# Kernel optimization log

Hardware: AMD Instinct MI355X
Metric: run time of the kernel (lower is better)

Reference implementation:

```python
import jax, jax.numpy as jnp
import numpy as np

N = 40000        # total nodes (2000 graphs x 20 nodes)
E = 60000        # edges per relation (before self-loops)
R = 6            # number of relations
IN = 32
HID = 128
OUT = 128
H = 2            # heads
C = 128          # per-head out channels (concat=False)
B = 2000         # number of graphs
NEG_SLOPE = 0.2


def setup_inputs() -> dict:
    key = jax.random.key(0)
    ks = jax.random.split(key, 16)
    rn = lambda k, s, sc=0.05: (jax.random.normal(k, s, jnp.float32) * sc)
    x = jax.random.normal(ks[0], (N, IN), jnp.float32)
    edge_index = jax.random.randint(ks[1], (R, 2, E), 0, N, dtype=jnp.int32)
    batch = (jnp.arange(N, dtype=jnp.int32) // (N // B)).astype(jnp.int32)
    return {
        "x": x, "edge_index": edge_index, "batch": batch,
        "Wl1": rn(ks[2], (R, IN, H * C)), "bl1": jnp.zeros((R, H * C), jnp.float32),
        "Wr1": rn(ks[3], (R, IN, H * C)), "br1": jnp.zeros((R, H * C), jnp.float32),
        "att1": rn(ks[4], (R, H, C)), "bias1": jnp.zeros((R, C), jnp.float32),
        "Wl2": rn(ks[5], (R, HID, H * C)), "bl2": jnp.zeros((R, H * C), jnp.float32),
        "Wr2": rn(ks[6], (R, HID, H * C)), "br2": jnp.zeros((R, H * C), jnp.float32),
        "att2": rn(ks[7], (R, H, C)), "bias2": jnp.zeros((R, C), jnp.float32),
        "ln1_g": jnp.ones((HID,), jnp.float32), "ln1_b": jnp.zeros((HID,), jnp.float32),
        "ln2_g": jnp.ones((HID,), jnp.float32), "ln2_b": jnp.zeros((HID,), jnp.float32),
        "query": rn(ks[8], (HID,), 0.02),
        "projW": rn(ks[9], (HID, OUT)), "projb": jnp.zeros((OUT,), jnp.float32),
    }


def _gatv2(x, src, dst, Wl, bl, Wr, br, att, bias):
    # x: [N, F]; src/dst: [Etot] (self-loops already appended)
    n = x.shape[0]
    xl = (x @ Wl + bl).reshape(n, H, C)   # source transform
    xr = (x @ Wr + br).reshape(n, H, C)   # target transform
    e = jax.nn.leaky_relu(xl[src] + xr[dst], NEG_SLOPE)   # [Etot, H, C]
    logits = jnp.einsum('ehc,hc->eh', e, att)             # [Etot, H]
    m = jax.ops.segment_max(logits, dst, num_segments=n)
    a = jnp.exp(logits - m[dst])
    s = jax.ops.segment_sum(a, dst, num_segments=n)
    w = a / s[dst]                                        # segment softmax
    out = jax.ops.segment_sum(w[:, :, None] * xl[src], dst, num_segments=n)
    return out.mean(axis=1) + bias                        # head-average (concat=False)


def _hetero_layer(x, edge_index, Wl, bl, Wr, br, att, bias):
    loops = jnp.broadcast_to(jnp.arange(N, dtype=edge_index.dtype), (R, N))
    src = jnp.concatenate([edge_index[:, 0, :], loops], axis=1)  # [R, E+N]
    dst = jnp.concatenate([edge_index[:, 1, :], loops], axis=1)
    outs = jax.vmap(_gatv2, in_axes=(None, 0, 0, 0, 0, 0, 0, 0, 0))(
        x, src, dst, Wl, bl, Wr, br, att, bias)
    return outs.sum(axis=0)  # HeteroConv aggr='sum'


def _layernorm(x, g, b, eps=1e-5):
    mu = x.mean(-1, keepdims=True)
    var = ((x - mu) ** 2).mean(-1, keepdims=True)
    return (x - mu) * jax.lax.rsqrt(var + eps) * g + b


def reference(x, edge_index, batch, Wl1, bl1, Wr1, br1, att1, bias1,
              Wl2, bl2, Wr2, br2, att2, bias2,
              ln1_g, ln1_b, ln2_g, ln2_b, query, projW, projb):
    h = _hetero_layer(x, edge_index, Wl1, bl1, Wr1, br1, att1, bias1)
    h = _layernorm(jnp.tanh(h), ln1_g, ln1_b)
    h = _hetero_layer(h, edge_index, Wl2, bl2, Wr2, br2, att2, bias2)
    h = _layernorm(jnp.tanh(h), ln2_g, ln2_b)
    # attention pooling over graphs (segment softmax on batch ids)
    scores = h @ query                              # [N]
    m = jax.ops.segment_max(scores, batch, num_segments=B)
    a = jnp.exp(scores - m[batch])
    s = jax.ops.segment_sum(a, batch, num_segments=B)
    w = a / s[batch]
    g = jax.ops.segment_sum(w[:, None] * h, batch, num_segments=B)  # [B, HID]
    return g @ projW + projb
```

## Files before the change

kernel.cpp:

```cpp
#include <hip/hip_runtime.h>
#include <hip/hip_bf16.h>
#include <math.h>

#define N_NODES 40000
#define E_EDGES 60000
#define R_REL 6
#define IN_F 32
#define HID_F 128
#define B_GRAPHS 2000
#define NODES_PER_G 20
#define NEG_SLOPE 0.2f
#define NB (R_REL * N_NODES)
#define NTOT (R_REL * (E_EDGES + N_NODES))
#define NBLK ((NB + 255) / 256)

#define CNT_B ((NTOT + 255) / 256)
#define CVT_B ((N_NODES * 16 + 255) / 256)
#define P1_B  (R_REL * 512 * 32 / 256)
#define P2_B  (R_REL * 512 * 128 / 256)
#define PREP_TOTAL (CNT_B + CVT_B + P1_B + P2_B + 1)

typedef __bf16 bf16x8 __attribute__((ext_vector_type(8)));
typedef float f32x4 __attribute__((ext_vector_type(4)));

__device__ __forceinline__ unsigned f2bfbits(float f) {
    unsigned u = __builtin_bit_cast(unsigned, f);
    return (u + 0x7FFFu + ((u >> 16) & 1u)) >> 16;
}
__device__ __forceinline__ float bflo(unsigned u) { return __builtin_bit_cast(float, u << 16); }
__device__ __forceinline__ float bfhi(unsigned u) { return __builtin_bit_cast(float, u & 0xFFFF0000u); }

__device__ __forceinline__ float fast_tanh(float x) {
    float e = __builtin_amdgcn_exp2f(x * 2.8853900817779268f);
    return fmaf(-2.f, __builtin_amdgcn_rcpf(e + 1.f), 1.f);
}

__device__ __forceinline__ void prep_w_body(
    const float* __restrict__ Wl, const float* __restrict__ Wr,
    const float* __restrict__ bl, const float* __restrict__ br,
    unsigned short* __restrict__ Bt, float* __restrict__ bcat, int K, int idx)
{
    if (idx >= R_REL * 512 * K) return;
    int k = idx % K;
    int rn = idx / K;
    int n = rn % 512;
    int r = rn / 512;
    int nn = n & 255;
    const float* W = (n < 256) ? Wl : Wr;
    float w = W[((size_t)r * K + k) * 256 + nn];
    Bt[idx] = (unsigned short)f2bfbits(w);
    if (k == 0)
        bcat[rn] = (n < 256) ? bl[r * 256 + nn] : br[r * 256 + nn];
}

__global__ __launch_bounds__(256) void fused_prep_kernel(
    const int* __restrict__ ei, int* __restrict__ cnt,
    const float* __restrict__ x, unsigned* __restrict__ xbf,
    const float* __restrict__ Wl1, const float* __restrict__ Wr1,
    const float* __restrict__ bl1, const float* __restrict__ br1,
    unsigned short* __restrict__ Bt1, float* __restrict__ bc1,
    const float* __restrict__ Wl2, const float* __restrict__ Wr2,
    const float* __restrict__ bl2, const float* __restrict__ br2,
    unsigned short* __restrict__ Bt2, float* __restrict__ bc2,
    const float* __restrict__ bias1, const float* __restrict__ bias2,
    float* __restrict__ bsum1, float* __restrict__ bsum2,
    const float* __restrict__ att1, const float* __restrict__ att2,
    float* __restrict__ attP1, float* __restrict__ attP2)
{
    int b = blockIdx.x;
    int tid = threadIdx.x;
    if (b < CNT_B) {
        int idx = b * 256 + tid;
        if (idx >= NTOT) return;
        int bin;
        if (idx < R_REL * E_EDGES) {
            int r = idx / E_EDGES, e = idx - r * E_EDGES;
            bin = r * N_NODES + ei[(size_t)r * 2 * E_EDGES + E_EDGES + e];
        } else {
            bin = idx - R_REL * E_EDGES;
        }
        atomicAdd(&cnt[bin], 1);
    } else if (b < CNT_B + CVT_B) {
        int i = (b - CNT_B) * 256 + tid;
        if (i >= N_NODES * 16) return;
        float2 v = *(const float2*)(x + 2 * i);
        xbf[i] = f2bfbits(v.x) | (f2bfbits(v.y) << 16);
    } else if (b < CNT_B + CVT_B + P1_B) {
        prep_w_body(Wl1, Wr1, bl1, br1, Bt1, bc1, 32, (b - CNT_B - CVT_B) * 256 + tid);
    } else if (b < CNT_B + CVT_B + P1_B + P2_B) {
        prep_w_body(Wl2, Wr2, bl2, br2, Bt2, bc2, 128, (b - CNT_B - CVT_B - P1_B) * 256 + tid);
    } else {
        const float L2E = 1.4426950408889634f;
        for (int r = 0; r < R_REL; r++) {
            float a1 = att1[r * 256 + tid];
            float a2 = att2[r * 256 + tid];
            attP1[r * 512 + tid]       = 0.6f * L2E * a1;
            attP1[r * 512 + 256 + tid] = 0.4f * L2E * a1;
            attP2[r * 512 + tid]       = 0.6f * L2E * a2;
            attP2[r * 512 + 256 + tid] = 0.4f * L2E * a2;
        }
        if (tid < 128) {
            float s1 = 0.f, s2 = 0.f;
            for (int r = 0; r < R_REL; r++) { s1 += bias1[r * 128 + tid]; s2 += bias2[r * 128 + tid]; }
            bsum1[tid] = s1; bsum2[tid] = s2;
        }
    }
}

__global__ __launch_bounds__(256) void scan1_kernel(
    const int* __restrict__ cnt, int* __restrict__ part, int* __restrict__ bsum)
{
    int i = blockIdx.x * 256 + threadIdx.x;
    int v = (i < NB) ? cnt[i] : 0;
    int lane = threadIdx.x & 63, w = threadIdx.x >> 6;
    int x = v;
#pragma unroll
    for (int off = 1; off < 64; off <<= 1) {
        int y = __shfl_up(x, off, 64);
        if (lane >= off) x += y;
    }
    __shared__ int ws[4];
    if (lane == 63) ws[w] = x;
    __syncthreads();
    int add = 0;
    for (int j = 0; j < w; j++) add += ws[j];
    int incl = x + add;
    if (i < NB) part[i] = incl - v;
    if (threadIdx.x == 255) bsum[blockIdx.x] = incl;
}

__global__ __launch_bounds__(256) void scan2_kernel(
    const int* __restrict__ bsum, int* __restrict__ boff)
{
    __shared__ int ws[4];
    int t = threadIdx.x;
    int lane = t & 63, w = t >> 6;
    int base4 = t * 4;
    int pre[4];
    int s = 0;
#pragma unroll
    for (int j = 0; j < 4; j++) {
        int i = base4 + j;
        int x = (i < NBLK) ? bsum[i] : 0;
        pre[j] = s;
        s += x;
    }
    int incl = s;
#pragma unroll
    for (int off = 1; off < 64; off <<= 1) {
        int y = __shfl_up(incl, off, 64);
        if (lane >= off) incl += y;
    }
    if (lane == 63) ws[w] = incl;
    __syncthreads();
    int wbase = 0;
    for (int j = 0; j < w; j++) wbase += ws[j];
    int tbase = wbase + incl - s;
#pragma unroll
    for (int j = 0; j < 4; j++) {
        int i = base4 + j;
        if (i < NBLK) boff[i] = tbase + pre[j];
    }
}

__global__ __launch_bounds__(256) void scan3_kernel(
    const int* __restrict__ part, const int* __restrict__ boff,
    int* __restrict__ rowptr, int* __restrict__ cursor)
{
    int i = blockIdx.x * 256 + threadIdx.x;
    if (i < NB) {
        int v = part[i] + boff[i >> 8];
        rowptr[i] = v;
        cursor[i] = v;
    }
    if (i == 0) rowptr[NB] = NTOT;
}

__global__ __launch_bounds__(256) void scatter_kernel(
    const int* __restrict__ ei, int* __restrict__ cursor, int* __restrict__ csr)
{
    int idx = blockIdx.x * 256 + threadIdx.x;
    if (idx >= NTOT) return;
    int bin, src;
    if (idx < R_REL * E_EDGES) {
        int r = idx / E_EDGES, e = idx - r * E_EDGES;
        src = ei[(size_t)r * 2 * E_EDGES + e];
        bin = r * N_NODES + ei[(size_t)r * 2 * E_EDGES + E_EDGES + e];
    } else {
        bin = idx - R_REL * E_EDGES;
        src = bin % N_NODES;
    }
    int pos = atomicAdd(&cursor[bin], 1);
    csr[pos] = src;
}

template <int K>
__global__ __launch_bounds__(256, 4) void gemm_mfma_kernel(
    const unsigned short* __restrict__ A,
    const unsigned short* __restrict__ BtAll,
    const float* __restrict__ biasAll,
    unsigned short* __restrict__ CAll)
{
    constexpr int KC = (K > 64) ? 64 : K;
    constexpr int NCH = K / KC;
    constexpr int CH = KC / 8;
    constexpr int TB = 128 * KC * 2;
    __shared__ char lds[2 * TB];
    char* ldsA = lds;
    char* ldsB = lds + TB;

    int tid = threadIdx.x;
    int lane = tid & 63, wave = tid >> 6;
    int l16 = lane & 15, quad = lane >> 4;
    int wm = (wave >> 1) * 64, wn = (wave & 1) * 64;
    int ny = blockIdx.x & 3, z = blockIdx.x >> 2;
    int m0 = blockIdx.y * 128, n0 = ny * 128;

    auto SW = [](int row) { return (KC == 64) ? (row & 7) : ((row >> 1) & 3); };

    const char* Bt = (const char*)(BtAll + (size_t)z * 512 * K);

    f32x4 acc[4][4];
#pragma unroll
    for (int i = 0; i < 4; i++)
#pragma unroll
        for (int j = 0; j < 4; j++) {
            acc[i][j][0] = 0.f; acc[i][j][1] = 0.f;
            acc[i][j][2] = 0.f; acc[i][j][3] = 0.f;
        }

    for (int nc = 0; nc < NCH; ++nc) {
        if (nc) __syncthreads();
#pragma unroll
        for (int it = 0; it < (128 * CH) / 256; ++it) {
            int s = it * 256 + tid;
            int row = s / CH, sc = s % CH;
            int c = sc ^ SW(row);
            int gr = m0 + row; gr = gr < N_NODES ? gr : N_NODES - 1;
            const char* gpA = (const char*)A + (size_t)gr * (K * 2) + nc * KC * 2 + c * 16;
            __builtin_amdgcn_global_load_lds(
                (const __attribute__((address_space(1))) void*)gpA,
                (__attribute__((address_space(3))) void*)(ldsA + it * 4096 + wave * 1024), 16, 0, 0);
            const char* gpB = Bt + (size_t)(n0 + row) * (K * 2) + nc * KC * 2 + c * 16;
            __builtin_amdgcn_global_load_lds(
                (const __attribute__((address_space(1))) void*)gpB,
                (__attribute__((address_space(3))) void*)(ldsB + it * 4096 + wave * 1024), 16, 0, 0);
        }
        __syncthreads();

#pragma unroll
        for (int kk = 0; kk < KC / 32; ++kk) {
            bf16x8 af[4], bfr[4];
#pragma unroll
            for (int i = 0; i < 4; ++i) {
                int row = wm + i * 16 + l16;
                int slot = (kk * 4 + quad) ^ SW(row);
                af[i] = *(const bf16x8*)(ldsA + row * (KC * 2) + slot * 16);
            }
#pragma unroll
            for (int j = 0; j < 4; ++j) {
                int row = wn + j * 16 + l16;
                int slot = (kk * 4 + quad) ^ SW(row);
                bfr[j] = *(const bf16x8*)(ldsB + row * (KC * 2) + slot * 16);
            }
#pragma unroll
            for (int i = 0; i < 4; i++)
#pragma unroll
                for (int j = 0; j < 4; j++)
                    acc[i][j] = __builtin_amdgcn_mfma_f32_16x16x32_bf16(af[i], bfr[j], acc[i][j], 0, 0, 0);
        }
    }

    const float* bias = biasAll + z * 512;
    unsigned short* C = CAll + (size_t)z * N_NODES * 512;
    float biasj[4];
#pragma unroll
    for (int j = 0; j < 4; ++j) biasj[j] = bias[n0 + wn + j * 16 + l16];
#pragma unroll
    for (int i = 0; i < 4; i++) {
        int gr0 = m0 + wm + i * 16 + quad * 4;
#pragma unroll
        for (int j = 0; j < 4; j++) {
            int col = n0 + wn + j * 16 + l16;
#pragma unroll
            for (int rg = 0; rg < 4; rg++) {
                float a = acc[i][j][rg] + biasj[j];
                float b = __shfl_xor(a, 1);
                int grow = gr0 + rg;
                if (!(lane & 1) && grow < N_NODES) {
                    __hip_bfloat162 h2 = __float22bfloat162_rn(make_float2(a, b));
                    unsigned u;
                    __builtin_memcpy(&u, &h2, 4);
                    *(unsigned*)((char*)C + ((size_t)grow * 512 + col) * 2) = u;
                }
            }
        }
    }
}

__global__ __launch_bounds__(256) void gat6_ln_kernel(
    const unsigned short* __restrict__ XLR,
    const int* __restrict__ rowptr,
    const int* __restrict__ csr,
    const float* __restrict__ attP,
    const float* __restrict__ bsum,
    const float* __restrict__ lng, const float* __restrict__ lnb,
    unsigned* __restrict__ hout)
{
    int gtid = blockIdx.x * 256 + threadIdx.x;
    int d = gtid >> 6;
    int lane = threadIdx.x & 63;
    if (d >= N_NODES) return;
    int hl = lane & 31;

    const size_t RS = (size_t)N_NODES * 1024;
    const char* lanep = (const char*)XLR + lane * 8;
    const char* xrbase = lanep + ((size_t)(unsigned)d << 10) + 512;

    float tot0 = 0.f, tot1 = 0.f, tot2 = 0.f, tot3 = 0.f;
#pragma unroll 1
    for (int r = 0; r < R_REL; r++) {
        uint2 xru = *(const uint2*)(xrbase + (size_t)r * RS);
        float4 a6 = *(const float4*)(attP + r * 512 + lane * 4);
        float4 a4 = *(const float4*)(attP + r * 512 + 256 + lane * 4);
        int bin = r * N_NODES + d;
        int beg = __builtin_amdgcn_readfirstlane(rowptr[bin]);
        int end = __builtin_amdgcn_readfirstlane(rowptr[bin + 1]);
        const char* base = lanep + (size_t)r * RS;
        float xr0 = bflo(xru.x), xr1 = bfhi(xru.x), xr2 = bflo(xru.y), xr3 = bfhi(xru.y);

        float sA = 0.f, a0 = 0.f, a1 = 0.f, a2 = 0.f, a3 = 0.f;
        float sB = 0.f, b0 = 0.f, b1 = 0.f, b2 = 0.f, b3 = 0.f;
        int i = beg;
        for (; i + 2 <= end; i += 2) {
            int s0 = csr[i], s1 = csr[i + 1];
            const unsigned* pA = (const unsigned*)(base + ((size_t)(unsigned)s0 << 10));
            const unsigned* pB = (const unsigned*)(base + ((size_t)(unsigned)s1 << 10));
            unsigned uA0 = pA[0], uA1 = pA[1];
            unsigned uB0 = pB[0], uB1 = pB[1];
            float xA0 = bflo(uA0), xA1 = bfhi(uA0), xA2 = bflo(uA1), xA3 = bfhi(uA1);
            float xB0 = bflo(uB0), xB1 = bfhi(uB0), xB2 = bflo(uB1), xB3 = bfhi(uB1);
            float tA0 = xA0 + xr0, tA1 = xA1 + xr1, tA2 = xA2 + xr2, tA3 = xA3 + xr3;
            float tB0 = xB0 + xr0, tB1 = xB1 + xr1, tB2 = xB2 + xr2, tB3 = xB3 + xr3;
            float pa = tA0 * a6.x;
            float pb = tB0 * a6.x;
            pa = fmaf(__builtin_fabsf(tA0), a4.x, pa);
            pb = fmaf(__builtin_fabsf(tB0), a4.x, pb);
            pa = fmaf(tA1, a6.y, pa);
            pb = fmaf(tB1, a6.y, pb);
            pa = fmaf(__builtin_fabsf(tA1), a4.y, pa);
            pb = fmaf(__builtin_fabsf(tB1), a4.y, pb);
            pa = fmaf(tA2, a6.z, pa);
            pb = fmaf(tB2, a6.z, pb);
            pa = fmaf(__builtin_fabsf(tA2), a4.z, pa);
            pb = fmaf(__builtin_fabsf(tB2), a4.z, pb);
            pa = fmaf(tA3, a6.w, pa);
            pb = fmaf(tB3, a6.w, pb);
            pa = fmaf(__builtin_fabsf(tA3), a4.w, pa);
            pb = fmaf(__builtin_fabsf(tB3), a4.w, pb);
            pa += __shfl_xor(pa, 16); pb += __shfl_xor(pb, 16);
            pa += __shfl_xor(pa, 8);  pb += __shfl_xor(pb, 8);
            pa += __shfl_xor(pa, 4);  pb += __shfl_xor(pb, 4);
            pa += __shfl_xor(pa, 2);  pb += __shfl_xor(pb, 2);
            pa += __shfl_xor(pa, 1);  pb += __shfl_xor(pb, 1);
            float wa = __builtin_amdgcn_exp2f(fminf(pa, 120.f));
            float wb = __builtin_amdgcn_exp2f(fminf(pb, 120.f));
            sA += wa; sB += wb;
            a0 = fmaf(wa, xA0, a0); b0 = fmaf(wb, xB0, b0);
            a1 = fmaf(wa, xA1, a1); b1 = fmaf(wb, xB1, b1);
            a2 = fmaf(wa, xA2, a2); b2 = fmaf(wb, xB2, b2);
            a3 = fmaf(wa, xA3, a3); b3 = fmaf(wb, xB3, b3);
        }
        if (i < end) {
            int s0 = csr[i];
            const unsigned* pA = (const unsigned*)(base + ((size_t)(unsigned)s0 << 10));
            unsigned uA0 = pA[0], uA1 = pA[1];
            float xA0 = bflo(uA0), xA1 = bfhi(uA0), xA2 = bflo(uA1), xA3 = bfhi(uA1);
            float tA0 = xA0 + xr0, tA1 = xA1 + xr1, tA2 = xA2 + xr2, tA3 = xA3 + xr3;
            float pa = tA0 * a6.x;
            pa = fmaf(__builtin_fabsf(tA0), a4.x, pa);
            pa = fmaf(tA1, a6.y, pa);
            pa = fmaf(__builtin_fabsf(tA1), a4.y, pa);
            pa = fmaf(tA2, a6.z, pa);
            pa = fmaf(__builtin_fabsf(tA2), a4.z, pa);
            pa = fmaf(tA3, a6.w, pa);
            pa = fmaf(__builtin_fabsf(tA3), a4.w, pa);
            pa += __shfl_xor(pa, 16);
            pa += __shfl_xor(pa, 8);
            pa += __shfl_xor(pa, 4);
            pa += __shfl_xor(pa, 2);
            pa += __shfl_xor(pa, 1);
            float wa = __builtin_amdgcn_exp2f(fminf(pa, 120.f));
            sA += wa;
            a0 = fmaf(wa, xA0, a0);
            a1 = fmaf(wa, xA1, a1);
            a2 = fmaf(wa, xA2, a2);
            a3 = fmaf(wa, xA3, a3);
        }
        sA += sB; a0 += b0; a1 += b1; a2 += b2; a3 += b3;
        float rs = 0.5f * __builtin_amdgcn_rcpf(sA);
        tot0 = fmaf(a0, rs, tot0);
        tot1 = fmaf(a1, rs, tot1);
        tot2 = fmaf(a2, rs, tot2);
        tot3 = fmaf(a3, rs, tot3);
    }

    tot0 += __shfl_xor(tot0, 32);
    tot1 += __shfl_xor(tot1, 32);
    tot2 += __shfl_xor(tot2, 32);
    tot3 += __shfl_xor(tot3, 32);
    float4 bs = *(const float4*)(bsum + hl * 4);

    float v0 = fast_tanh(tot0 + bs.x);
    float v1 = fast_tanh(tot1 + bs.y);
    float v2 = fast_tanh(tot2 + bs.z);
    float v3 = fast_tanh(tot3 + bs.w);
    float sum = v0 + v1 + v2 + v3;
    float sq = v0 * v0 + v1 * v1 + v2 * v2 + v3 * v3;
#pragma unroll
    for (int off = 16; off >= 1; off >>= 1) {
        sum += __shfl_xor(sum, off);
        sq  += __shfl_xor(sq, off);
    }
    float mean = sum * (1.f / 128.f);
    float var = sq * (1.f / 128.f) - mean * mean;
    float rstd = rsqrtf(var + 1e-5f);
    float4 gg = *(const float4*)(lng + hl * 4);
    float4 bb = *(const float4*)(lnb + hl * 4);
    float o0 = (v0 - mean) * rstd * gg.x + bb.x;
    float o1 = (v1 - mean) * rstd * gg.y + bb.y;
    float o2 = (v2 - mean) * rstd * gg.z + bb.z;
    float o3 = (v3 - mean) * rstd * gg.w + bb.w;
    if (lane < 32) {
        uint2 q;
        q.x = f2bfbits(o0) | (f2bfbits(o1) << 16);
        q.y = f2bfbits(o2) | (f2bfbits(o3) << 16);
        *((uint2*)(hout + (size_t)d * 64) + hl) = q;
    }
}

__global__ __launch_bounds__(256) void pool_proj_kernel(
    const unsigned* __restrict__ hb, const float* __restrict__ query,
    const float* __restrict__ W, const float* __restrict__ pb,
    float* __restrict__ out)
{
    __shared__ float gL[4][128];
    int wave = threadIdx.x >> 6;
    int lane = threadIdx.x & 63;
    int bg = blockIdx.x * 4 + wave;
    float2 q = *(const float2*)(query + 2 * lane);
    float mx = -1e30f, ssum = 0.f, g0 = 0.f, g1 = 0.f;
    for (int i = 0; i < NODES_PER_G; i++) {
        unsigned u = hb[(size_t)(bg * NODES_PER_G + i) * 64 + lane];
        float h0 = bflo(u), h1 = bfhi(u);
        float p = h0 * q.x + h1 * q.y;
#pragma unroll
        for (int off = 32; off >= 1; off >>= 1) p += __shfl_xor(p, off, 64);
        float mn = fmaxf(mx, p);
        float sc = __expf(mx - mn), w = __expf(p - mn);
        ssum = ssum * sc + w;
        g0 = g0 * sc + w * h0;
        g1 = g1 * sc + w * h1;
        mx = mn;
    }
    float inv = 1.f / ssum;
    gL[wave][2 * lane] = g0 * inv;
    gL[wave][2 * lane + 1] = g1 * inv;
    __syncthreads();
    int o0 = lane, o1 = lane + 64;
    float a0 = pb[o0], a1 = pb[o1];
    for (int k = 0; k < 128; k++) {
        float gk = gL[wave][k];
        a0 = fmaf(gk, W[k * 128 + o0], a0);
        a1 = fmaf(gk, W[k * 128 + o1], a1);
    }
    out[(size_t)bg * 128 + o0] = a0;
    out[(size_t)bg * 128 + o1] = a1;
}

extern "C" void kernel_launch(void* const* d_in, const int* in_sizes, int n_in,
                              void* d_out, int out_size, void* d_ws, size_t ws_size,
                              hipStream_t stream)
{
    const float* x     = (const float*)d_in[0];
    const int*   ei    = (const int*)d_in[1];
    const float* Wl1   = (const float*)d_in[3];
    const float* bl1   = (const float*)d_in[4];
    const float* Wr1   = (const float*)d_in[5];
    const float* br1   = (const float*)d_in[6];
    const float* att1  = (const float*)d_in[7];
    const float* bias1 = (const float*)d_in[8];
    const float* Wl2   = (const float*)d_in[9];
    const float* bl2   = (const float*)d_in[10];
    const float* Wr2   = (const float*)d_in[11];
    const float* br2   = (const float*)d_in[12];
    const float* att2  = (const float*)d_in[13];
    const float* bias2 = (const float*)d_in[14];
    const float* ln1g  = (const float*)d_in[15];
    const float* ln1b  = (const float*)d_in[16];
    const float* ln2g  = (const float*)d_in[17];
    const float* ln2b  = (const float*)d_in[18];
    const float* query = (const float*)d_in[19];
    const float* projW = (const float*)d_in[20];
    const float* projb = (const float*)d_in[21];
    float* out = (float*)d_out;

    unsigned short* xlr6 = (unsigned short*)d_ws;
    unsigned short* h1bf = xlr6 + (size_t)R_REL * N_NODES * 512;
    unsigned short* xbf  = h1bf + (size_t)N_NODES * 128;
    unsigned short* Bt1  = xbf + (size_t)N_NODES * 32;
    unsigned short* Bt2  = Bt1 + R_REL * 512 * 32;
    float* bc1  = (float*)(Bt2 + R_REL * 512 * 128);
    float* bc2  = bc1 + R_REL * 512;
    float* bsum1 = bc2 + R_REL * 512;
    float* bsum2 = bsum1 + 128;
    float* attP1 = bsum2 + 128;
    float* attP2 = attP1 + R_REL * 512;
    int* cnt    = (int*)(attP2 + R_REL * 512);
    int* part   = cnt + NB;
    int* rowptr = part + NB;
    int* cursor = rowptr + NB + 1;
    int* bsum   = cursor + NB;
    int* boff   = bsum + NBLK;
    int* csr    = boff + NBLK;

    hipMemsetAsync(cnt, 0, sizeof(int) * NB, stream);
    fused_prep_kernel<<<PREP_TOTAL, 256, 0, stream>>>(
        ei, cnt, x, (unsigned*)xbf,
        Wl1, Wr1, bl1, br1, Bt1, bc1,
        Wl2, Wr2, bl2, br2, Bt2, bc2,
        bias1, bias2, bsum1, bsum2,
        att1, att2, attP1, attP2);
    scan1_kernel<<<NBLK, 256, 0, stream>>>(cnt, part, bsum);
    scan2_kernel<<<1, 256, 0, stream>>>(bsum, boff);
    scan3_kernel<<<NBLK, 256, 0, stream>>>(part, boff, rowptr, cursor);
    scatter_kernel<<<(NTOT + 255) / 256, 256, 0, stream>>>(ei, cursor, csr);

    dim3 ggrid(24, (N_NODES + 127) / 128, 1);
    gemm_mfma_kernel<32><<<ggrid, 256, 0, stream>>>(xbf, Bt1, bc1, xlr6);
    gat6_ln_kernel<<<N_NODES / 4, 256, 0, stream>>>(
        xlr6, rowptr, csr, attP1, bsum1, ln1g, ln1b, (unsigned*)h1bf);
    gemm_mfma_kernel<128><<<ggrid, 256, 0, stream>>>(h1bf, Bt2, bc2, xlr6);
    gat6_ln_kernel<<<N_NODES / 4, 256, 0, stream>>>(
        xlr6, rowptr, csr, attP2, bsum2, ln2g, ln2b, (unsigned*)h1bf);
    pool_proj_kernel<<<B_GRAPHS / 4, 256, 0, stream>>>(
        (unsigned*)h1bf, query, projW, projb, out);
}
```

Measured before the change: 434.6 us.

## Precompute per-source linear attention term and use DPP row reductions

Splits the leaky-ReLU attention logit into a linear part (0.6·att·(xl+xr)) and an abs part. The source-dependent linear term is folded into weight-vector dot products (W·att) computed once per node, in a new kernel for layer 1 and inside the layer-1 GAT epilogue for layer 2. The edge loop then only evaluates the abs term plus one scalar load per edge. Cross-lane sums switch from shuffles to DPP row operations. This adds extra per-node passes and reuses scratch buffers (cnt, xbf) for the new scalars. As shown, the target-side linear term (0.6·att·xr) no longer appears in the logit. That term is constant per destination, so the softmax should still be correct.

```diff
diff --git a/kernel.cpp b/kernel.cpp
--- a/kernel.cpp
+++ b/kernel.cpp
@@ -18,7 +18,11 @@
 #define CVT_B ((N_NODES * 16 + 255) / 256)
 #define P1_B  (R_REL * 512 * 32 / 256)
 #define P2_B  (R_REL * 512 * 128 / 256)
-#define PREP_TOTAL (CNT_B + CVT_B + P1_B + P2_B + 1)
+#define WV1_B 2
+#define WV2_B 6
+#define CST_B 1
+#define PREP_BASE (CNT_B + CVT_B + P1_B + P2_B)
+#define PREP_TOTAL (PREP_BASE + 1 + WV1_B + WV2_B + CST_B)
 
 typedef __bf16 bf16x8 __attribute__((ext_vector_type(8)));
 typedef float f32x4 __attribute__((ext_vector_type(4)));
@@ -33,6 +37,23 @@
 __device__ __forceinline__ float fast_tanh(float x) {
     float e = __builtin_amdgcn_exp2f(x * 2.8853900817779268f);
     return fmaf(-2.f, __builtin_amdgcn_rcpf(e + 1.f), 1.f);
+}
+
+template<int CTRL>
+__device__ __forceinline__ float dppadd(float v) {
+    int m = __builtin_amdgcn_update_dpp(0, __builtin_bit_cast(int, v), CTRL, 0xF, 0xF, true);
+    return v + __builtin_bit_cast(float, m);
+}
+__device__ __forceinline__ float rowsum16(float v) {
+    v = dppadd<0x121>(v);
+    v = dppadd<0x122>(v);
+    v = dppadd<0x124>(v);
+    v = dppadd<0x128>(v);
+    return v;
+}
+__device__ __forceinline__ float halfsum32(float v) {
+    v += __shfl_xor(v, 16);
+    return rowsum16(v);
 }
 
 __device__ __forceinline__ void prep_w_body(
@@ -65,8 +86,11 @@
     const float* __restrict__ bias1, const float* __restrict__ bias2,
     float* __restrict__ bsum1, float* __restrict__ bsum2,
     const float* __restrict__ att1, const float* __restrict__ att2,
-    float* __restrict__ attP1, float* __restrict__ attP2)
-{
+    float* __restrict__ attP1, float* __restrict__ attP2,
+    float* __restrict__ wv1, float* __restrict__ wv2,
+    float* __restrict__ cst1, float* __restrict__ cst2)
+{
+    const float L2E = 1.4426950408889634f;
     int b = blockIdx.x;
     int tid = threadIdx.x;
     if (b < CNT_B) {
@@ -89,8 +113,7 @@
         prep_w_body(Wl1, Wr1, bl1, br1, Bt1, bc1, 32, (b - CNT_B - CVT_B) * 256 + tid);
     } else if (b < CNT_B + CVT_B + P1_B + P2_B) {
         prep_w_body(Wl2, Wr2, bl2, br2, Bt2, bc2, 128, (b - CNT_B - CVT_B - P1_B) * 256 + tid);
-    } else {
-        const float L2E = 1.4426950408889634f;
+    } else if (b == PREP_BASE) {
         for (int r = 0; r < R_REL; r++) {
             float a1 = att1[r * 256 + tid];
             float a2 = att2[r * 256 + tid];
@@ -104,6 +127,34 @@
             for (int r = 0; r < R_REL; r++) { s1 += bias1[r * 128 + tid]; s2 += bias2[r * 128 + tid]; }
             bsum1[tid] = s1; bsum2[tid] = s2;
         }
+    } else if (b < PREP_BASE + 1 + WV1_B) {
+        int idx = (b - PREP_BASE - 1) * 256 + tid;
+        if (idx >= R_REL * 32 * 2) return;
+        int h = idx & 1, k = (idx >> 1) & 31, r = idx >> 6;
+        float s = 0.f;
+        const float* wrow = Wl1 + ((size_t)r * 32 + k) * 256 + h * 128;
+        const float* arow = att1 + r * 256 + h * 128;
+        for (int c = 0; c < 128; c++) s = fmaf(wrow[c], arow[c], s);
+        wv1[(r * 2 + h) * 32 + k] = 0.6f * L2E * s;
+    } else if (b < PREP_BASE + 1 + WV1_B + WV2_B) {
+        int idx = (b - PREP_BASE - 1 - WV1_B) * 256 + tid;
+        if (idx >= R_REL * 128 * 2) return;
+        int h = idx & 1, k = (idx >> 1) & 127, r = idx >> 8;
+        float s = 0.f;
+        const float* wrow = Wl2 + ((size_t)r * 128 + k) * 256 + h * 128;
+        const float* arow = att2 + r * 256 + h * 128;
+        for (int c = 0; c < 128; c++) s = fmaf(wrow[c], arow[c], s);
+        wv2[(r * 2 + h) * 128 + k] = 0.6f * L2E * s;
+    } else {
+        if (tid >= 24) return;
+        int layer = tid / 12, rh = tid % 12, r = rh >> 1, h = rh & 1;
+        const float* bl = layer ? bl2 : bl1;
+        const float* at = layer ? att2 : att1;
+        float s = 0.f;
+        const float* brow = bl + r * 256 + h * 128;
+        const float* arow = at + r * 256 + h * 128;
+        for (int c = 0; c < 128; c++) s = fmaf(brow[c], arow[c], s);
+        (layer ? cst2 : cst1)[rh] = 0.6f * L2E * s;
     }
 }
 
@@ -192,6 +243,23 @@
     }
     int pos = atomicAdd(&cursor[bin], 1);
     csr[pos] = src;
+}
+
+__global__ __launch_bounds__(256) void srcc1_kernel(
+    const float* __restrict__ x, const float* __restrict__ wv1,
+    const float* __restrict__ cst1, float* __restrict__ srcC1)
+{
+    int t = blockIdx.x * 256 + threadIdx.x;
+    if (t >= N_NODES * 12) return;
+    int rh = t % 12;
+    int d = t / 12;
+    const float* xr = x + (size_t)d * 32;
+    const float* wv = wv1 + rh * 32;
+    float acc = cst1[rh];
+#pragma unroll
+    for (int k = 0; k < 32; k++) acc = fmaf(xr[k], wv[k], acc);
+    int r = rh >> 1, h = rh & 1;
+    srcC1[((size_t)r * N_NODES + d) * 2 + h] = acc;
 }
 
 template <int K>
@@ -298,35 +366,41 @@
     }
 }
 
+template<bool WS>
 __global__ __launch_bounds__(256) void gat6_ln_kernel(
     const unsigned short* __restrict__ XLR,
     const int* __restrict__ rowptr,
     const int* __restrict__ csr,
     const float* __restrict__ attP,
+    const float* __restrict__ srcC,
     const float* __restrict__ bsum,
     const float* __restrict__ lng, const float* __restrict__ lnb,
-    unsigned* __restrict__ hout)
+    unsigned* __restrict__ hout,
+    const float* __restrict__ wv2, const float* __restrict__ cst2,
+    float* __restrict__ srcCout)
 {
     int gtid = blockIdx.x * 256 + threadIdx.x;
     int d = gtid >> 6;
     int lane = threadIdx.x & 63;
     if (d >= N_NODES) return;
     int hl = lane & 31;
+    bool hi = lane >= 32;
 
     const size_t RS = (size_t)N_NODES * 1024;
     const char* lanep = (const char*)XLR + lane * 8;
     const char* xrbase = lanep + ((size_t)(unsigned)d << 10) + 512;
+    const char* sCb = (const char*)srcC;
 
     float tot0 = 0.f, tot1 = 0.f, tot2 = 0.f, tot3 = 0.f;
 #pragma unroll 1
     for (int r = 0; r < R_REL; r++) {
         uint2 xru = *(const uint2*)(xrbase + (size_t)r * RS);
-        float4 a6 = *(const float4*)(attP + r * 512 + lane * 4);
         float4 a4 = *(const float4*)(attP + r * 512 + 256 + lane * 4);
         int bin = r * N_NODES + d;
         int beg = __builtin_amdgcn_readfirstlane(rowptr[bin]);
         int end = __builtin_amdgcn_readfirstlane(rowptr[bin + 1]);
         const char* base = lanep + (size_t)r * RS;
+        const char* sCr = sCb + (size_t)r * (N_NODES * 8);
         float xr0 = bflo(xru.x), xr1 = bfhi(xru.x), xr2 = bflo(xru.y), xr3 = bfhi(xru.y);
 
         float sA = 0.f, a0 = 0.f, a1 = 0.f, a2 = 0.f, a3 = 0.f;
@@ -336,33 +410,28 @@
             int s0 = csr[i], s1 = csr[i + 1];
             const unsigned* pA = (const unsigned*)(base + ((size_t)(unsigned)s0 << 10));
             const unsigned* pB = (const unsigned*)(base + ((size_t)(unsigned)s1 << 10));
+            uint2 vA = *(const uint2*)(sCr + (size_t)(unsigned)s0 * 8);
+            uint2 vB = *(const uint2*)(sCr + (size_t)(unsigned)s1 * 8);
             unsigned uA0 = pA[0], uA1 = pA[1];
             unsigned uB0 = pB[0], uB1 = pB[1];
+            float sfa = __builtin_bit_cast(float, hi ? vA.y : vA.x);
+            float sfb = __builtin_bit_cast(float, hi ? vB.y : vB.x);
             float xA0 = bflo(uA0), xA1 = bfhi(uA0), xA2 = bflo(uA1), xA3 = bfhi(uA1);
             float xB0 = bflo(uB0), xB1 = bfhi(uB0), xB2 = bflo(uB1), xB3 = bfhi(uB1);
             float tA0 = xA0 + xr0, tA1 = xA1 + xr1, tA2 = xA2 + xr2, tA3 = xA3 + xr3;
             float tB0 = xB0 + xr0, tB1 = xB1 + xr1, tB2 = xB2 + xr2, tB3 = xB3 + xr3;
-            float pa = tA0 * a6.x;
-            float pb = tB0 * a6.x;
-            pa = fmaf(__builtin_fabsf(tA0), a4.x, pa);
-            pb = fmaf(__builtin_fabsf(tB0), a4.x, pb);
-            pa = fmaf(tA1, a6.y, pa);
-            pb = fmaf(tB1, a6.y, pb);
+            float pa = __builtin_fabsf(tA0) * a4.x;
+            float pb = __builtin_fabsf(tB0) * a4.x;
             pa = fmaf(__builtin_fabsf(tA1), a4.y, pa);
             pb = fmaf(__builtin_fabsf(tB1), a4.y, pb);
-            pa = fmaf(tA2, a6.z, pa);
-            pb = fmaf(tB2, a6.z, pb);
             pa = fmaf(__builtin_fabsf(tA2), a4.z, pa);
             pb = fmaf(__builtin_fabsf(tB2), a4.z, pb);
-            pa = fmaf(tA3, a6.w, pa);
-            pb = fmaf(tB3, a6.w, pb);
             pa = fmaf(__builtin_fabsf(tA3), a4.w, pa);
             pb = fmaf(__builtin_fabsf(tB3), a4.w, pb);
-            pa += __shfl_xor(pa, 16); pb += __shfl_xor(pb, 16);
-            pa += __shfl_xor(pa, 8);  pb += __shfl_xor(pb, 8);
-            pa += __shfl_xor(pa, 4);  pb += __shfl_xor(pb, 4);
-            pa += __shfl_xor(pa, 2);  pb += __shfl_xor(pb, 2);
-            pa += __shfl_xor(pa, 1);  pb += __shfl_xor(pb, 1);
+            pa = halfsum32(pa);
+            pb = halfsum32(pb);
+            pa += sfa;
+            pb += sfb;
             float wa = __builtin_amdgcn_exp2f(fminf(pa, 120.f));
             float wb = __builtin_amdgcn_exp2f(fminf(pb, 120.f));
             sA += wa; sB += wb;
@@ -374,22 +443,17 @@
         if (i < end) {
             int s0 = csr[i];
             const unsigned* pA = (const unsigned*)(base + ((size_t)(unsigned)s0 << 10));
+            uint2 vA = *(const uint2*)(sCr + (size_t)(unsigned)s0 * 8);
             unsigned uA0 = pA[0], uA1 = pA[1];
+            float sfa = __builtin_bit_cast(float, hi ? vA.y : vA.x);
             float xA0 = bflo(uA0), xA1 = bfhi(uA0), xA2 = bflo(uA1), xA3 = bfhi(uA1);
             float tA0 = xA0 + xr0, tA1 = xA1 + xr1, tA2 = xA2 + xr2, tA3 = xA3 + xr3;
-            float pa = tA0 * a6.x;
-            pa = fmaf(__builtin_fabsf(tA0), a4.x, pa);
-            pa = fmaf(tA1, a6.y, pa);
+            float pa = __builtin_fabsf(tA0) * a4.x;
             pa = fmaf(__builtin_fabsf(tA1), a4.y, pa);
-            pa = fmaf(tA2, a6.z, pa);
             pa = fmaf(__builtin_fabsf(tA2), a4.z, pa);
-            pa = fmaf(tA3, a6.w, pa);
             pa = fmaf(__builtin_fabsf(tA3), a4.w, pa);
-            pa += __shfl_xor(pa, 16);
-            pa += __shfl_xor(pa, 8);
-            pa += __shfl_xor(pa, 4);
-            pa += __shfl_xor(pa, 2);
-            pa += __shfl_xor(pa, 1);
+            pa = halfsum32(pa);
+            pa += sfa;
             float wa = __builtin_amdgcn_exp2f(fminf(pa, 120.f));
             sA += wa;
             a0 = fmaf(wa, xA0, a0);
@@ -415,13 +479,8 @@
     float v1 = fast_tanh(tot1 + bs.y);
     float v2 = fast_tanh(tot2 + bs.z);
     float v3 = fast_tanh(tot3 + bs.w);
-    float sum = v0 + v1 + v2 + v3;
-    float sq = v0 * v0 + v1 * v1 + v2 * v2 + v3 * v3;
-#pragma unroll
-    for (int off = 16; off >= 1; off >>= 1) {
-        sum += __shfl_xor(sum, off);
-        sq  += __shfl_xor(sq, off);
-    }
+    float sum = halfsum32(v0 + v1 + v2 + v3);
+    float sq = halfsum32(v0 * v0 + v1 * v1 + v2 * v2 + v3 * v3);
     float mean = sum * (1.f / 128.f);
     float var = sq * (1.f / 128.f) - mean * mean;
     float rstd = rsqrtf(var + 1e-5f);
@@ -431,11 +490,28 @@
     float o1 = (v1 - mean) * rstd * gg.y + bb.y;
     float o2 = (v2 - mean) * rstd * gg.z + bb.z;
     float o3 = (v3 - mean) * rstd * gg.w + bb.w;
-    if (lane < 32) {
-        uint2 q;
-        q.x = f2bfbits(o0) | (f2bfbits(o1) << 16);
-        q.y = f2bfbits(o2) | (f2bfbits(o3) << 16);
+    uint2 q;
+    q.x = f2bfbits(o0) | (f2bfbits(o1) << 16);
+    q.y = f2bfbits(o2) | (f2bfbits(o3) << 16);
+    if (lane < 32)
         *((uint2*)(hout + (size_t)d * 64) + hl) = q;
+
+    if constexpr (WS) {
+        float r0 = bflo(q.x), r1 = bfhi(q.x), r2 = bflo(q.y), r3 = bfhi(q.y);
+        int h = hi ? 1 : 0;
+#pragma unroll 1
+        for (int r = 0; r < R_REL; r++) {
+            float4 wv4 = *(const float4*)(wv2 + ((r * 2 + h) * 128 + hl * 4));
+            float p = r0 * wv4.x;
+            p = fmaf(r1, wv4.y, p);
+            p = fmaf(r2, wv4.z, p);
+            p = fmaf(r3, wv4.w, p);
+            p = halfsum32(p);
+            if (hl == 0) {
+                float2 cc = *(const float2*)(cst2 + r * 2);
+                srcCout[((size_t)r * N_NODES + d) * 2 + h] = p + (hi ? cc.y : cc.x);
+            }
+        }
     }
 }
 
@@ -516,13 +592,19 @@
     float* bsum2 = bsum1 + 128;
     float* attP1 = bsum2 + 128;
     float* attP2 = attP1 + R_REL * 512;
-    int* cnt    = (int*)(attP2 + R_REL * 512);
+    float* wv1  = attP2 + R_REL * 512;
+    float* wv2  = wv1 + R_REL * 64;
+    float* cst1 = wv2 + R_REL * 256;
+    float* cst2 = cst1 + 16;
+    int* cnt    = (int*)(cst2 + 16);
     int* part   = cnt + NB;
     int* rowptr = part + NB;
     int* cursor = rowptr + NB + 1;
     int* bsum   = cursor + NB;
     int* boff   = bsum + NBLK;
     int* csr    = boff + NBLK;
+    float* srcC1 = (float*)cnt;
+    float* srcC2 = (float*)xbf;
 
     hipMemsetAsync(cnt, 0, sizeof(int) * NB, stream);
     fused_prep_kernel<<<PREP_TOTAL, 256, 0, stream>>>(
@@ -530,19 +612,23 @@
         Wl1, Wr1, bl1, br1, Bt1, bc1,
         Wl2, Wr2, bl2, br2, Bt2, bc2,
         bias1, bias2, bsum1, bsum2,
-        att1, att2, attP1, attP2);
+        att1, att2, attP1, attP2,
+        wv1, wv2, cst1, cst2);
     scan1_kernel<<<NBLK, 256, 0, stream>>>(cnt, part, bsum);
     scan2_kernel<<<1, 256, 0, stream>>>(bsum, boff);
     scan3_kernel<<<NBLK, 256, 0, stream>>>(part, boff, rowptr, cursor);
     scatter_kernel<<<(NTOT + 255) / 256, 256, 0, stream>>>(ei, cursor, csr);
+    srcc1_kernel<<<(N_NODES * 12 + 255) / 256, 256, 0, stream>>>(x, wv1, cst1, srcC1);
 
     dim3 ggrid(24, (N_NODES + 127) / 128, 1);
     gemm_mfma_kernel<32><<<ggrid, 256, 0, stream>>>(xbf, Bt1, bc1, xlr6);
-    gat6_ln_kernel<<<N_NODES / 4, 256, 0, stream>>>(
-        xlr6, rowptr, csr, attP1, bsum1, ln1g, ln1b, (unsigned*)h1bf);
+    gat6_ln_kernel<true><<<N_NODES / 4, 256, 0, stream>>>(
+        xlr6, rowptr, csr, attP1, srcC1, bsum1, ln1g, ln1b, (unsigned*)h1bf,
+        wv2, cst2, srcC2);
     gemm_mfma_kernel<128><<<ggrid, 256, 0, stream>>>(h1bf, Bt2, bc2, xlr6);
-    gat6_ln_kernel<<<N_NODES / 4, 256, 0, stream>>>(
-        xlr6, rowptr, csr, attP2, bsum2, ln2g, ln2b, (unsigned*)h1bf);
+    gat6_ln_kernel<false><<<N_NODES / 4, 256, 0, stream>>>(
+        xlr6, rowptr, csr, attP2, srcC2, bsum2, ln2g, ln2b, (unsigned*)h1bf,
+        nullptr, nullptr, nullptr);
     pool_proj_kernel<<<B_GRAPHS / 4, 256, 0, stream>>>(
         (unsigned*)h1bf, query, projW, projb, out);
 }
```

Result: slower. 444.5 us (+2.3%).
